# Performance work log

Measured on AMD Instinct MI355X. Metric: run time of the kernel, lower is better.

Reference implementation:

```python
import jax, jax.numpy as jnp
import numpy as np

N = 20000; E = 320000; INPUT_DIM = 512; HIDDEN = 128; OUT_DIM = 64
ORIGIN = 256; PRETRAIN = 256; HEADS = 8; DK = 16; DC = 256
MAX_POS = 512; NTRAIN = 200000


def setup_inputs():
    ks = jax.random.split(jax.random.key(0), 24)
    def p(i, shape):
        return jax.random.normal(ks[i], shape, dtype=jnp.float32) * 0.05
    z = lambda n: jnp.zeros((n,), jnp.float32)
    return {
        "x": jax.random.normal(ks[0], (N, INPUT_DIM), dtype=jnp.float32),
        "train_sample": jax.random.randint(ks[1], (NTRAIN, 2), 0, N),
        "data_feature": jax.random.normal(ks[2], (N, INPUT_DIM), dtype=jnp.float32),
        "adj": jax.random.randint(ks[3], (2, E), 0, N),
        "positions": jax.random.randint(ks[4], (N,), 0, MAX_POS),
        "gcn_W": p(5, (INPUT_DIM, ORIGIN)), "gcn_b": z(ORIGIN),
        "gcnA2_W": p(6, (INPUT_DIM, PRETRAIN)), "gcnA2_b": z(PRETRAIN),
        "lin_W": p(7, (ORIGIN, HIDDEN)), "lin_b": z(HIDDEN),
        "tf_W": p(8, (PRETRAIN, HIDDEN)), "tf_b": z(HIDDEN),
        "tg_W": p(9, (PRETRAIN, HIDDEN)), "tg_b": z(HIDDEN),
        "Wq": p(10, (HIDDEN, HEADS * DK)), "bq": z(HEADS * DK),
        "Wk": p(11, (HIDDEN, HEADS * DK)), "bk": z(HEADS * DK),
        "Wv": p(12, (HIDDEN, HEADS * DK)), "bv": z(HEADS * DK),
        "Wo": p(13, (HEADS * DK, HIDDEN)), "bo": z(HIDDEN),
        "Ek": p(14, (DC, N)), "Ev": p(15, (DC, N)),
        "pos_emb": p(16, (MAX_POS, HIDDEN)),
        "tfa_W": p(17, (HIDDEN, OUT_DIM)), "tfa_b": z(OUT_DIM),
        "tga_W": p(18, (HIDDEN, OUT_DIM)), "tga_b": z(OUT_DIM),
    }


def _leaky(v):
    return jnp.where(v >= 0, v, 0.01 * v)


def _gcn(x, W, b, src, dst):
    # PyG GCNConv: add self-loops, symmetric D^-1/2 (A+I) D^-1/2 normalization
    h = x @ W                                   # [N, F_out]
    deg = jnp.ones((N,), x.dtype).at[dst].add(1.0)   # degree incl. self-loop
    dinv = jax.lax.rsqrt(deg)
    coef = (dinv[src] * dinv[dst])[:, None]
    agg = jax.ops.segment_sum(h[src] * coef, dst, num_segments=N)
    return agg + h * (dinv * dinv)[:, None] + b


def _attention(q_in, k_in, v_in, positions, pos_emb, Wq, bq, Wk, bk, Wv, bv, Wo, bo, Ek, Ev):
    # Compressed (Linformer-style) multi-head attention over the node axis:
    # keys/values projected from N nodes down to DC landmarks (d_c=d_c_prime=256).
    pe = pos_emb[positions]                     # [N, HIDDEN]
    q = ((q_in + pe) @ Wq + bq).reshape(N, HEADS, DK)
    k = (k_in + pe) @ Wk + bk                   # [N, HEADS*DK]
    v = v_in @ Wv + bv
    kc = (Ek @ k).reshape(DC, HEADS, DK)        # [DC, H, DK]
    vc = (Ev @ v).reshape(DC, HEADS, DK)
    scores = jnp.einsum("nhd,chd->hnc", q, kc) / (DK ** 0.5)
    w = jax.nn.softmax(scores, axis=-1)         # [H, N, DC]
    out = jnp.einsum("hnc,chd->nhd", w, vc).reshape(N, HEADS * DK)
    return out @ Wo + bo                        # [N, HIDDEN]


def reference(x, train_sample, data_feature, adj, positions,
              gcn_W, gcn_b, gcnA2_W, gcnA2_b, lin_W, lin_b,
              tf_W, tf_b, tg_W, tg_b,
              Wq, bq, Wk, bk, Wv, bv, Wo, bo, Ek, Ev, pos_emb,
              tfa_W, tfa_b, tga_W, tga_b):
    src, dst = adj[0], adj[1]
    x_g = jax.nn.sigmoid(_gcn(data_feature, gcn_W, gcn_b, src, dst))
    x_g = _leaky(x_g @ lin_W + lin_b)
    x_a = _gcn(data_feature, gcnA2_W, gcnA2_b, src, dst)
    tf_embed = _leaky(x_a @ tf_W + tf_b)
    target_embed = _leaky(x_a @ tg_W + tg_b)
    x_f = _attention(x_g, tf_embed, target_embed, positions, pos_emb,
                     Wq, bq, Wk, bk, Wv, bv, Wo, bo, Ek, Ev)
    tfa = _leaky(x_f @ tfa_W + tfa_b)
    tga = _leaky(x_f @ tga_W + tga_b)
    a = tfa[train_sample[:, 0]]
    b = tga[train_sample[:, 1]]
    dot = jnp.sum(a * b, axis=1)
    denom = jnp.maximum(jnp.linalg.norm(a, axis=1) * jnp.linalg.norm(b, axis=1), 1e-8)
    return (dot / denom)[:, None]                # [NTRAIN, 1]
```

## Files before the change

### kernel.cpp

```cpp
#include <hip/hip_runtime.h>
#include <hip/hip_bf16.h>

#define N_NODES 20000
#define E_EDGES 320000
#define NTRAIN  200000
#define KC_SPLITS 64

template<int PRE, int POST>
__global__ __launch_bounds__(256) void gemm_f32(
    const float* __restrict__ A, const float* __restrict__ W,
    const float* __restrict__ bias, float* __restrict__ C,
    int M, int K, int Nn,
    const int* __restrict__ positions, const float* __restrict__ pos_emb)
{
    __shared__ float As[16][68];
    __shared__ float Bs[16][64];

    const int t  = threadIdx.x;
    const int m0 = blockIdx.x * 64;
    const int n0 = blockIdx.y * 64;

    const int kl  = t & 15;
    const int ml  = t >> 4;
    const int nl  = t & 63;
    const int kl2 = t >> 6;
    const int tc  = t & 15;
    const int tr  = t >> 4;

    float acc[4][4] = {};

    for (int k0 = 0; k0 < K; k0 += 16) {
        #pragma unroll
        for (int i = 0; i < 4; i++) {
            int row = m0 + ml + i * 16;
            float v = 0.f;
            if (row < M) {
                v = A[(size_t)row * K + k0 + kl];
                if (PRE == 1) v = 1.f / (1.f + expf(-v));
                if (PRE == 2) v += pos_emb[(size_t)positions[row] * K + k0 + kl];
            }
            As[kl][ml + i * 16] = v;
        }
        #pragma unroll
        for (int i = 0; i < 4; i++) {
            int kk = kl2 * 4 + i;
            Bs[kk][nl] = W[(size_t)(k0 + kk) * Nn + n0 + nl];
        }
        __syncthreads();
        #pragma unroll
        for (int kk = 0; kk < 16; kk++) {
            float4 ra = *reinterpret_cast<const float4*>(&As[kk][tr * 4]);
            float4 rb = *reinterpret_cast<const float4*>(&Bs[kk][tc * 4]);
            float am[4] = {ra.x, ra.y, ra.z, ra.w};
            float bn[4] = {rb.x, rb.y, rb.z, rb.w};
            #pragma unroll
            for (int i = 0; i < 4; i++)
                #pragma unroll
                for (int j = 0; j < 4; j++)
                    acc[i][j] += am[i] * bn[j];
        }
        __syncthreads();
    }

    #pragma unroll
    for (int i = 0; i < 4; i++) {
        int row = m0 + tr * 4 + i;
        if (row >= M) continue;
        #pragma unroll
        for (int j = 0; j < 4; j++) {
            int col = n0 + tc * 4 + j;
            float v = acc[i][j] + (bias ? bias[col] : 0.f);
            if (POST == 1) v = (v >= 0.f) ? v : 0.01f * v;
            C[(size_t)row * Nn + col] = v;
        }
    }
}

template<int PRE, int POST>
__global__ __launch_bounds__(256) void gemm_f32_n128(
    const float* __restrict__ A, const float* __restrict__ W,
    const float* __restrict__ bias, float* __restrict__ C,
    int M, int K, int Nn,
    const int* __restrict__ positions, const float* __restrict__ pos_emb)
{
    __shared__ float As[16][68];
    __shared__ float Bs[16][144];

    const int t  = threadIdx.x;
    const int m0 = blockIdx.x * 64;
    const int n0 = blockIdx.y * 128;

    const int kl = t & 15;
    const int ml = t >> 4;
    const int nl = t & 127;
    const int kb = t >> 7;

    const int tc = t & 15;
    const int tr = t >> 4;
    const int bPhys = tc * 8 + (tc >> 2) * 4;

    float acc[4][8] = {};

    for (int k0 = 0; k0 < K; k0 += 16) {
        #pragma unroll
        for (int i = 0; i < 4; i++) {
            int row = m0 + ml + i * 16;
            float v = 0.f;
            if (row < M) {
                v = A[(size_t)row * K + k0 + kl];
                if (PRE == 1) v = 1.f / (1.f + expf(-v));
                if (PRE == 2) v += pos_emb[(size_t)positions[row] * K + k0 + kl];
            }
            As[kl][ml + i * 16] = v;
        }
        {
            int pc = nl + (nl >> 5) * 4;
            #pragma unroll
            for (int i = 0; i < 8; i++) {
                int kk = kb + i * 2;
                Bs[kk][pc] = W[(size_t)(k0 + kk) * Nn + n0 + nl];
            }
        }
        __syncthreads();
        #pragma unroll
        for (int kk = 0; kk < 16; kk++) {
            float4 ra  = *reinterpret_cast<const float4*>(&As[kk][tr * 4]);
            float4 rb0 = *reinterpret_cast<const float4*>(&Bs[kk][bPhys]);
            float4 rb1 = *reinterpret_cast<const float4*>(&Bs[kk][bPhys + 4]);
            float am[4] = {ra.x, ra.y, ra.z, ra.w};
            float bn[8] = {rb0.x, rb0.y, rb0.z, rb0.w, rb1.x, rb1.y, rb1.z, rb1.w};
            #pragma unroll
            for (int i = 0; i < 4; i++)
                #pragma unroll
                for (int j = 0; j < 8; j++)
                    acc[i][j] += am[i] * bn[j];
        }
        __syncthreads();
    }

    #pragma unroll
    for (int i = 0; i < 4; i++) {
        int row = m0 + tr * 4 + i;
        if (row >= M) continue;
        float4 o0, o1;
        float* po0 = (float*)&o0;
        float* po1 = (float*)&o1;
        #pragma unroll
        for (int j = 0; j < 4; j++) {
            float v = acc[i][j] + (bias ? bias[n0 + tc * 8 + j] : 0.f);
            if (POST == 1) v = (v >= 0.f) ? v : 0.01f * v;
            po0[j] = v;
            float w = acc[i][j + 4] + (bias ? bias[n0 + tc * 8 + 4 + j] : 0.f);
            if (POST == 1) w = (w >= 0.f) ? w : 0.01f * w;
            po1[j] = w;
        }
        *reinterpret_cast<float4*>(&C[(size_t)row * Nn + n0 + tc * 8])     = o0;
        *reinterpret_cast<float4*>(&C[(size_t)row * Nn + n0 + tc * 8 + 4]) = o1;
    }
}

__global__ void zero_kernel(float* __restrict__ p, int n)
{
    int i = blockIdx.x * 256 + threadIdx.x;
    if (i < n) p[i] = 0.f;
}

__global__ void csr_count(const int* __restrict__ dst, int* __restrict__ count)
{
    int e = blockIdx.x * 256 + threadIdx.x;
    int stride = gridDim.x * 256;
    for (; e < E_EDGES; e += stride)
        atomicAdd(&count[dst[e]], 1);
}

__global__ __launch_bounds__(1024) void csr_scan(
    const int* __restrict__ count, int* __restrict__ rowptr,
    int* __restrict__ cursor, float* __restrict__ dinv)
{
    __shared__ int s[1024];
    const int t = threadIdx.x;
    int carry = 0;
    for (int base = 0; base < N_NODES; base += 1024) {
        int i = base + t;
        int v = (i < N_NODES) ? count[i] : 0;
        if (i < N_NODES) dinv[i] = rsqrtf(1.f + (float)v);
        s[t] = v;
        __syncthreads();
        for (int off = 1; off < 1024; off <<= 1) {
            int add = (t >= off) ? s[t - off] : 0;
            __syncthreads();
            s[t] += add;
            __syncthreads();
        }
        int incl  = s[t];
        int total = s[1023];
        if (i < N_NODES) {
            rowptr[i] = carry + incl - v;
            cursor[i] = carry + incl - v;
        }
        carry += total;
        __syncthreads();
    }
    if (t == 0) rowptr[N_NODES] = carry;
}

__global__ void csr_fill(const int* __restrict__ src, const int* __restrict__ dst,
                         int* __restrict__ cursor, int* __restrict__ srcs)
{
    int e = blockIdx.x * 256 + threadIdx.x;
    int stride = gridDim.x * 256;
    for (; e < E_EDGES; e += stride) {
        int slot = atomicAdd(&cursor[dst[e]], 1);
        srcs[slot] = src[e];
    }
}

__global__ __launch_bounds__(256) void gcn_aggregate(
    const float* __restrict__ H1, const float* __restrict__ H2,
    const float* __restrict__ dinv,
    const int* __restrict__ rowptr, const int* __restrict__ srcs,
    const float* __restrict__ b1, const float* __restrict__ b2,
    float* __restrict__ O1, float* __restrict__ O2)
{
    const int n = blockIdx.x;
    const int f = threadIdx.x;
    const float dn = dinv[n];
    const size_t nidx = (size_t)n * 256 + f;

    float a1 = H1[nidx] * dn * dn + b1[f];
    float a2 = H2[nidx] * dn * dn + b2[f];

    const int e0 = rowptr[n];
    const int e1 = rowptr[n + 1];
    for (int e = e0; e < e1; e++) {
        int s = srcs[e];
        float c = dinv[s] * dn;
        size_t si = (size_t)s * 256 + f;
        a1 += H1[si] * c;
        a2 += H2[si] * c;
    }
    O1[nidx] = a1;
    O2[nidx] = a2;
}

__global__ __launch_bounds__(256) void kcvc_kernel(
    const float* __restrict__ Ek, const float* __restrict__ Ev,
    const float* __restrict__ kin, const float* __restrict__ vin,
    float* __restrict__ partial)
{
    const float* E = blockIdx.z ? Ev  : Ek;
    const float* X = blockIdx.z ? vin : kin;

    const int c0 = blockIdx.x * 128;
    const int per = 320;
    const int nStart = blockIdx.y * per;
    const int nEnd   = min(nStart + per, N_NODES);

    __shared__ float Es[32][144];
    __shared__ float Xs[32][144];

    const int t  = threadIdx.x;
    const int tc = t & 15;
    const int td = t >> 4;
    const int ePhys = tc * 8 + (tc >> 2) * 4;
    const int xPhys = td * 8 + (td >> 2) * 4;

    float acc[8][8] = {};

    for (int nb = nStart; nb < nEnd; nb += 32) {
        const int nc = min(32, nEnd - nb);

        {
            int cl  = t >> 1;
            int pc  = cl + (cl >> 5) * 4;
            int nnb = (t & 1) * 16;
            const float* srcp = &E[(size_t)(c0 + cl) * N_NODES + nb + nnb];
            if (nc == 32) {
                #pragma unroll
                for (int i = 0; i < 4; i++) {
                    float4 v = *reinterpret_cast<const float4*>(&srcp[i * 4]);
                    Es[nnb + i * 4 + 0][pc] = v.x;
                    Es[nnb + i * 4 + 1][pc] = v.y;
                    Es[nnb + i * 4 + 2][pc] = v.z;
                    Es[nnb + i * 4 + 3][pc] = v.w;
                }
            } else {
                for (int i = 0; i < 16; i++) {
                    int nn = nnb + i;
                    Es[nn][pc] = (nn < nc) ? srcp[i] : 0.f;
                }
            }
        }
        {
            #pragma unroll
            for (int i = 0; i < 4; i++) {
                int g  = t + i * 256;
                int nn = g >> 5;
                int d0 = (g & 31) * 4;
                int pd = d0 + (d0 >> 5) * 4;
                if (nn < nc) {
                    float4 v = *reinterpret_cast<const float4*>(&X[(size_t)(nb + nn) * 128 + d0]);
                    Xs[nn][pd + 0] = v.x; Xs[nn][pd + 1] = v.y;
                    Xs[nn][pd + 2] = v.z; Xs[nn][pd + 3] = v.w;
                } else {
                    Xs[nn][pd + 0] = 0.f; Xs[nn][pd + 1] = 0.f;
                    Xs[nn][pd + 2] = 0.f; Xs[nn][pd + 3] = 0.f;
                }
            }
        }
        __syncthreads();

        #pragma unroll 2
        for (int nn = 0; nn < 32; nn++) {
            float4 e0 = *reinterpret_cast<const float4*>(&Es[nn][ePhys]);
            float4 e1 = *reinterpret_cast<const float4*>(&Es[nn][ePhys + 4]);
            float4 x0 = *reinterpret_cast<const float4*>(&Xs[nn][xPhys]);
            float4 x1 = *reinterpret_cast<const float4*>(&Xs[nn][xPhys + 4]);
            float ev[8] = {e0.x, e0.y, e0.z, e0.w, e1.x, e1.y, e1.z, e1.w};
            float xv[8] = {x0.x, x0.y, x0.z, x0.w, x1.x, x1.y, x1.z, x1.w};
            #pragma unroll
            for (int ci = 0; ci < 8; ci++)
                #pragma unroll
                for (int dj = 0; dj < 8; dj++)
                    acc[ci][dj] += ev[ci] * xv[dj];
        }
        __syncthreads();
    }

    float* pb = partial + ((size_t)(blockIdx.z * KC_SPLITS + blockIdx.y)) * 32768;
    #pragma unroll
    for (int ci = 0; ci < 8; ci++) {
        int c = c0 + tc * 8 + ci;
        float4 v0 = {acc[ci][0], acc[ci][1], acc[ci][2], acc[ci][3]};
        float4 v1 = {acc[ci][4], acc[ci][5], acc[ci][6], acc[ci][7]};
        *reinterpret_cast<float4*>(&pb[(size_t)c * 128 + td * 8])     = v0;
        *reinterpret_cast<float4*>(&pb[(size_t)c * 128 + td * 8 + 4]) = v1;
    }
}

__global__ __launch_bounds__(256) void kcvc_reduce(
    const float* __restrict__ partial, float* __restrict__ out)
{
    int i4  = blockIdx.x * 256 + threadIdx.x;
    int mat = i4 >> 13;
    int off = (i4 & 8191) * 4;
    const float* p = partial + (size_t)mat * KC_SPLITS * 32768 + off;
    float4 acc = {0.f, 0.f, 0.f, 0.f};
    #pragma unroll 8
    for (int s = 0; s < KC_SPLITS; s++) {
        float4 v = *reinterpret_cast<const float4*>(p + (size_t)s * 32768);
        acc.x += v.x; acc.y += v.y; acc.z += v.z; acc.w += v.w;
    }
    *reinterpret_cast<float4*>(out + (size_t)mat * 32768 + off) = acc;
}

__global__ __launch_bounds__(256) void attn_kernel(
    const float* __restrict__ q, const float* __restrict__ kc,
    const float* __restrict__ vc, float* __restrict__ outp)
{
    __shared__ float q_s[16][132];
    __shared__ float kc_s[16][272];
    __shared__ float vc_s[256][20];
    __shared__ float w_s[16][264];

    const int t    = threadIdx.x;
    const int n0   = blockIdx.x * 16;
    const int node = t >> 4;
    const int tn   = t & 15;

    {
        const float* qp = q + (size_t)n0 * 128;
        #pragma unroll
        for (int i = 0; i < 2; i++) {
            int idx = t * 8 + i * 4;
            float4 v = *reinterpret_cast<const float4*>(&qp[idx]);
            *reinterpret_cast<float4*>(&q_s[idx >> 7][idx & 127]) = v;
        }
    }

    for (int h = 0; h < 8; h++) {
        __syncthreads();
        {
            const float* kp = &kc[(size_t)t * 128 + h * 16];
            float4 a0 = *reinterpret_cast<const float4*>(kp);
            float4 a1 = *reinterpret_cast<const float4*>(kp + 4);
            float4 a2 = *reinterpret_cast<const float4*>(kp + 8);
            float4 a3 = *reinterpret_cast<const float4*>(kp + 12);
            kc_s[ 0][t] = a0.x; kc_s[ 1][t] = a0.y; kc_s[ 2][t] = a0.z; kc_s[ 3][t] = a0.w;
            kc_s[ 4][t] = a1.x; kc_s[ 5][t] = a1.y; kc_s[ 6][t] = a1.z; kc_s[ 7][t] = a1.w;
            kc_s[ 8][t] = a2.x; kc_s[ 9][t] = a2.y; kc_s[10][t] = a2.z; kc_s[11][t] = a2.w;
            kc_s[12][t] = a3.x; kc_s[13][t] = a3.y; kc_s[14][t] = a3.z; kc_s[15][t] = a3.w;
            const float* vp = &vc[(size_t)t * 128 + h * 16];
            *reinterpret_cast<float4*>(&vc_s[t][ 0]) = *reinterpret_cast<const float4*>(vp);
            *reinterpret_cast<float4*>(&vc_s[t][ 4]) = *reinterpret_cast<const float4*>(vp + 4);
            *reinterpret_cast<float4*>(&vc_s[t][ 8]) = *reinterpret_cast<const float4*>(vp + 8);
            *reinterpret_cast<float4*>(&vc_s[t][12]) = *reinterpret_cast<const float4*>(vp + 12);
        }
        __syncthreads();

        float qr[16];
        #pragma unroll
        for (int d = 0; d < 16; d++) qr[d] = q_s[node][h * 16 + d];

        float sv[16];
        #pragma unroll
        for (int j = 0; j < 16; j++) {
            int c = tn + 16 * j;
            float a = 0.f;
            #pragma unroll
            for (int d = 0; d < 16; d++)
                a += qr[d] * kc_s[d][c];
            sv[j] = a * 0.25f;
        }

        float m = sv[0];
        #pragma unroll
        for (int j = 1; j < 16; j++) m = fmaxf(m, sv[j]);
        #pragma unroll
        for (int off = 8; off > 0; off >>= 1)
            m = fmaxf(m, __shfl_xor(m, off));

        float sum = 0.f;
        #pragma unroll
        for (int j = 0; j < 16; j++) {
            sv[j] = expf(sv[j] - m);
            sum += sv[j];
        }
        #pragma unroll
        for (int off = 8; off > 0; off >>= 1)
            sum += __shfl_xor(sum, off);
        float inv = 1.0f / sum;

        #pragma unroll
        for (int j = 0; j < 16; j++)
            w_s[node][tn + 16 * j] = sv[j] * inv;
        __syncthreads();

        float acc0 = 0.f, acc1 = 0.f, acc2 = 0.f, acc3 = 0.f;
        #pragma unroll 4
        for (int cb = 0; cb < 64; cb++) {
            int c = cb * 4;
            float4 w4 = *reinterpret_cast<const float4*>(&w_s[node][c]);
            acc0 += w4.x * vc_s[c + 0][tn];
            acc1 += w4.y * vc_s[c + 1][tn];
            acc2 += w4.z * vc_s[c + 2][tn];
            acc3 += w4.w * vc_s[c + 3][tn];
        }
        outp[(size_t)(n0 + node) * 128 + h * 16 + tn] = (acc0 + acc1) + (acc2 + acc3);
    }
}

__global__ __launch_bounds__(256) void cosine_kernel(
    const float* __restrict__ tfa, const float* __restrict__ tga,
    const int* __restrict__ ts, float* __restrict__ out)
{
    const int w    = threadIdx.x >> 6;
    const int lane = threadIdx.x & 63;
    const int t    = blockIdx.x * 4 + w;
    if (t >= NTRAIN) return;

    int i = ts[2 * t];
    int j = ts[2 * t + 1];
    float a = tfa[(size_t)i * 64 + lane];
    float b = tga[(size_t)j * 64 + lane];
    float da = a * b, na = a * a, nb = b * b;
    #pragma unroll
    for (int off = 32; off > 0; off >>= 1) {
        da += __shfl_xor(da, off);
        na += __shfl_xor(na, off);
        nb += __shfl_xor(nb, off);
    }
    if (lane == 0)
        out[t] = da / fmaxf(sqrtf(na) * sqrtf(nb), 1e-8f);
}

extern "C" void kernel_launch(void* const* d_in, const int* in_sizes, int n_in,
                              void* d_out, int out_size, void* d_ws, size_t ws_size,
                              hipStream_t stream)
{
    const int*   ts    = (const int*)  d_in[1];
    const float* X     = (const float*)d_in[2];
    const int*   adj   = (const int*)  d_in[3];
    const int*   pos   = (const int*)  d_in[4];
    const float* gcn_W = (const float*)d_in[5];
    const float* gcn_b = (const float*)d_in[6];
    const float* gA2_W = (const float*)d_in[7];
    const float* gA2_b = (const float*)d_in[8];
    const float* lin_W = (const float*)d_in[9];
    const float* lin_b = (const float*)d_in[10];
    const float* tf_W  = (const float*)d_in[11];
    const float* tf_b  = (const float*)d_in[12];
    const float* tg_W  = (const float*)d_in[13];
    const float* tg_b  = (const float*)d_in[14];
    const float* Wq    = (const float*)d_in[15];
    const float* bq    = (const float*)d_in[16];
    const float* Wk    = (const float*)d_in[17];
    const float* bk    = (const float*)d_in[18];
    const float* Wv    = (const float*)d_in[19];
    const float* bv    = (const float*)d_in[20];
    const float* Wo    = (const float*)d_in[21];
    const float* bo    = (const float*)d_in[22];
    const float* Ek    = (const float*)d_in[23];
    const float* Ev    = (const float*)d_in[24];
    const float* pemb  = (const float*)d_in[25];
    const float* tfaW  = (const float*)d_in[26];
    const float* tfab  = (const float*)d_in[27];
    const float* tgaW  = (const float*)d_in[28];
    const float* tgab  = (const float*)d_in[29];

    const int* src = adj;
    const int* dst = adj + E_EDGES;

    float* ws  = (float*)d_ws;
    float* H1  = ws;
    float* H2  = H1 + 5120000;
    float* O1  = H2 + 5120000;
    float* O2  = O1 + 5120000;
    float* dinv = O2 + 5120000;
    float* kc  = dinv + 20000;
    float* vc  = kc + 32768;
    int*   count  = (int*)(vc + 32768);
    int*   rowptr = count + 20000;
    int*   cursor = rowptr + 20001;
    int*   srcs   = cursor + 20000;
    float* xg   = H1;
    float* tfe  = H1 + 2560000;
    float* tge  = H2;
    float* qb   = H2 + 2560000;
    float* kb   = O1;
    float* vb   = O1 + 2560000;
    float* attn = O2;
    float* xf   = O2 + 2560000;
    float* tfa  = H1;
    float* tga  = H1 + 1280000;
    float* partial = H1;

    dim3 blk(256);
    const int MB = (N_NODES + 63) / 64;

    gemm_f32_n128<0,0><<<dim3(MB,2), blk, 0, stream>>>(X, gcn_W, nullptr, H1, N_NODES, 512, 256, nullptr, nullptr);
    gemm_f32_n128<0,0><<<dim3(MB,2), blk, 0, stream>>>(X, gA2_W, nullptr, H2, N_NODES, 512, 256, nullptr, nullptr);

    zero_kernel<<<(20000 + 255) / 256, blk, 0, stream>>>((float*)count, 20000);
    csr_count<<<1250, blk, 0, stream>>>(dst, count);
    csr_scan<<<1, 1024, 0, stream>>>(count, rowptr, cursor, dinv);
    csr_fill<<<1250, blk, 0, stream>>>(src, dst, cursor, srcs);

    gcn_aggregate<<<N_NODES, blk, 0, stream>>>(H1, H2, dinv, rowptr, srcs,
                                               gcn_b, gA2_b, O1, O2);

    gemm_f32_n128<1,1><<<dim3(MB,1), blk, 0, stream>>>(O1, lin_W, lin_b, xg, N_NODES, 256, 128, nullptr, nullptr);
    gemm_f32_n128<0,1><<<dim3(MB,1), blk, 0, stream>>>(O2, tf_W, tf_b, tfe, N_NODES, 256, 128, nullptr, nullptr);
    gemm_f32_n128<0,1><<<dim3(MB,1), blk, 0, stream>>>(O2, tg_W, tg_b, tge, N_NODES, 256, 128, nullptr, nullptr);

    gemm_f32_n128<2,0><<<dim3(MB,1), blk, 0, stream>>>(xg,  Wq, bq, qb, N_NODES, 128, 128, pos, pemb);
    gemm_f32_n128<2,0><<<dim3(MB,1), blk, 0, stream>>>(tfe, Wk, bk, kb, N_NODES, 128, 128, pos, pemb);
    gemm_f32_n128<0,0><<<dim3(MB,1), blk, 0, stream>>>(tge, Wv, bv, vb, N_NODES, 128, 128, nullptr, nullptr);

    kcvc_kernel<<<dim3(2, KC_SPLITS, 2), blk, 0, stream>>>(Ek, Ev, kb, vb, partial);
    kcvc_reduce<<<64, blk, 0, stream>>>(partial, kc);

    attn_kernel<<<1250, blk, 0, stream>>>(qb, kc, vc, attn);

    gemm_f32_n128<0,0><<<dim3(MB,1), blk, 0, stream>>>(attn, Wo, bo, xf, N_NODES, 128, 128, nullptr, nullptr);

    gemm_f32<0,1><<<dim3(MB,1), blk, 0, stream>>>(xf, tfaW, tfab, tfa, N_NODES, 128, 64, nullptr, nullptr);
    gemm_f32<0,1><<<dim3(MB,1), blk, 0, stream>>>(xf, tgaW, tgab, tga, N_NODES, 128, 64, nullptr, nullptr);

    cosine_kernel<<<NTRAIN / 4, blk, 0, stream>>>(tfa, tga, ts, (float*)d_out);
}
```

Baseline: 1.076 ms.

## Retile kcvc to 64-row blocks and register-tile attention scores

```diff
diff --git a/kernel.cpp b/kernel.cpp
--- a/kernel.cpp
+++ b/kernel.cpp
@@ -251,45 +251,32 @@
     const float* E = blockIdx.z ? Ev  : Ek;
     const float* X = blockIdx.z ? vin : kin;
 
-    const int c0 = blockIdx.x * 128;
+    const int c0 = blockIdx.x * 64;
     const int per = 320;
     const int nStart = blockIdx.y * per;
     const int nEnd   = min(nStart + per, N_NODES);
 
-    __shared__ float Es[32][144];
+    __shared__ float Es[32][68];
     __shared__ float Xs[32][144];
 
     const int t  = threadIdx.x;
     const int tc = t & 15;
     const int td = t >> 4;
-    const int ePhys = tc * 8 + (tc >> 2) * 4;
     const int xPhys = td * 8 + (td >> 2) * 4;
 
-    float acc[8][8] = {};
+    float acc[4][8] = {};
 
     for (int nb = nStart; nb < nEnd; nb += 32) {
-        const int nc = min(32, nEnd - nb);
-
         {
-            int cl  = t >> 1;
-            int pc  = cl + (cl >> 5) * 4;
-            int nnb = (t & 1) * 16;
+            int cl  = t >> 2;
+            int nnb = (t & 3) * 8;
             const float* srcp = &E[(size_t)(c0 + cl) * N_NODES + nb + nnb];
-            if (nc == 32) {
-                #pragma unroll
-                for (int i = 0; i < 4; i++) {
-                    float4 v = *reinterpret_cast<const float4*>(&srcp[i * 4]);
-                    Es[nnb + i * 4 + 0][pc] = v.x;
-                    Es[nnb + i * 4 + 1][pc] = v.y;
-                    Es[nnb + i * 4 + 2][pc] = v.z;
-                    Es[nnb + i * 4 + 3][pc] = v.w;
-                }
-            } else {
-                for (int i = 0; i < 16; i++) {
-                    int nn = nnb + i;
-                    Es[nn][pc] = (nn < nc) ? srcp[i] : 0.f;
-                }
-            }
+            float4 v0 = *reinterpret_cast<const float4*>(&srcp[0]);
+            float4 v1 = *reinterpret_cast<const float4*>(&srcp[4]);
+            Es[nnb + 0][cl] = v0.x; Es[nnb + 1][cl] = v0.y;
+            Es[nnb + 2][cl] = v0.z; Es[nnb + 3][cl] = v0.w;
+            Es[nnb + 4][cl] = v1.x; Es[nnb + 5][cl] = v1.y;
+            Es[nnb + 6][cl] = v1.z; Es[nnb + 7][cl] = v1.w;
         }
         {
             #pragma unroll
@@ -298,28 +285,22 @@
                 int nn = g >> 5;
                 int d0 = (g & 31) * 4;
                 int pd = d0 + (d0 >> 5) * 4;
-                if (nn < nc) {
-                    float4 v = *reinterpret_cast<const float4*>(&X[(size_t)(nb + nn) * 128 + d0]);
-                    Xs[nn][pd + 0] = v.x; Xs[nn][pd + 1] = v.y;
-                    Xs[nn][pd + 2] = v.z; Xs[nn][pd + 3] = v.w;
-                } else {
-                    Xs[nn][pd + 0] = 0.f; Xs[nn][pd + 1] = 0.f;
-                    Xs[nn][pd + 2] = 0.f; Xs[nn][pd + 3] = 0.f;
-                }
+                float4 v = *reinterpret_cast<const float4*>(&X[(size_t)(nb + nn) * 128 + d0]);
+                Xs[nn][pd + 0] = v.x; Xs[nn][pd + 1] = v.y;
+                Xs[nn][pd + 2] = v.z; Xs[nn][pd + 3] = v.w;
             }
         }
         __syncthreads();
 
         #pragma unroll 2
         for (int nn = 0; nn < 32; nn++) {
-            float4 e0 = *reinterpret_cast<const float4*>(&Es[nn][ePhys]);
-            float4 e1 = *reinterpret_cast<const float4*>(&Es[nn][ePhys + 4]);
+            float4 e4 = *reinterpret_cast<const float4*>(&Es[nn][tc * 4]);
             float4 x0 = *reinterpret_cast<const float4*>(&Xs[nn][xPhys]);
             float4 x1 = *reinterpret_cast<const float4*>(&Xs[nn][xPhys + 4]);
-            float ev[8] = {e0.x, e0.y, e0.z, e0.w, e1.x, e1.y, e1.z, e1.w};
+            float ev[4] = {e4.x, e4.y, e4.z, e4.w};
             float xv[8] = {x0.x, x0.y, x0.z, x0.w, x1.x, x1.y, x1.z, x1.w};
             #pragma unroll
-            for (int ci = 0; ci < 8; ci++)
+            for (int ci = 0; ci < 4; ci++)
                 #pragma unroll
                 for (int dj = 0; dj < 8; dj++)
                     acc[ci][dj] += ev[ci] * xv[dj];
@@ -327,10 +308,10 @@
         __syncthreads();
     }
 
-    float* pb = partial + ((size_t)(blockIdx.z * KC_SPLITS + blockIdx.y)) * 32768;
+    float* pb = partial + (size_t)(blockIdx.z * KC_SPLITS + blockIdx.y) * 32768;
     #pragma unroll
-    for (int ci = 0; ci < 8; ci++) {
-        int c = c0 + tc * 8 + ci;
+    for (int ci = 0; ci < 4; ci++) {
+        int c = c0 + tc * 4 + ci;
         float4 v0 = {acc[ci][0], acc[ci][1], acc[ci][2], acc[ci][3]};
         float4 v1 = {acc[ci][4], acc[ci][5], acc[ci][6], acc[ci][7]};
         *reinterpret_cast<float4*>(&pb[(size_t)c * 128 + td * 8])     = v0;
@@ -359,12 +340,14 @@
     const float* __restrict__ vc, float* __restrict__ outp)
 {
     __shared__ float q_s[16][132];
-    __shared__ float kc_s[16][272];
-    __shared__ float vc_s[256][20];
-    __shared__ float w_s[16][264];
+    __shared__ float kc_s[16][260];
+    __shared__ float vc_s[16][260];
+    __shared__ float w_s[16][260];
 
     const int t    = threadIdx.x;
     const int n0   = blockIdx.x * 16;
+    const int ng   = t >> 6;
+    const int tc2  = t & 63;
     const int node = t >> 4;
     const int tn   = t & 15;
 
@@ -391,62 +374,84 @@
             kc_s[ 8][t] = a2.x; kc_s[ 9][t] = a2.y; kc_s[10][t] = a2.z; kc_s[11][t] = a2.w;
             kc_s[12][t] = a3.x; kc_s[13][t] = a3.y; kc_s[14][t] = a3.z; kc_s[15][t] = a3.w;
             const float* vp = &vc[(size_t)t * 128 + h * 16];
-            *reinterpret_cast<float4*>(&vc_s[t][ 0]) = *reinterpret_cast<const float4*>(vp);
-            *reinterpret_cast<float4*>(&vc_s[t][ 4]) = *reinterpret_cast<const float4*>(vp + 4);
-            *reinterpret_cast<float4*>(&vc_s[t][ 8]) = *reinterpret_cast<const float4*>(vp + 8);
-            *reinterpret_cast<float4*>(&vc_s[t][12]) = *reinterpret_cast<const float4*>(vp + 12);
-        }
-        __syncthreads();
-
-        float qr[16];
-        #pragma unroll
-        for (int d = 0; d < 16; d++) qr[d] = q_s[node][h * 16 + d];
-
-        float sv[16];
-        #pragma unroll
-        for (int j = 0; j < 16; j++) {
-            int c = tn + 16 * j;
-            float a = 0.f;
-            #pragma unroll
-            for (int d = 0; d < 16; d++)
-                a += qr[d] * kc_s[d][c];
-            sv[j] = a * 0.25f;
-        }
-
-        float m = sv[0];
-        #pragma unroll
-        for (int j = 1; j < 16; j++) m = fmaxf(m, sv[j]);
-        #pragma unroll
-        for (int off = 8; off > 0; off >>= 1)
-            m = fmaxf(m, __shfl_xor(m, off));
-
-        float sum = 0.f;
-        #pragma unroll
-        for (int j = 0; j < 16; j++) {
-            sv[j] = expf(sv[j] - m);
-            sum += sv[j];
-        }
-        #pragma unroll
-        for (int off = 8; off > 0; off >>= 1)
-            sum += __shfl_xor(sum, off);
-        float inv = 1.0f / sum;
-
-        #pragma unroll
-        for (int j = 0; j < 16; j++)
-            w_s[node][tn + 16 * j] = sv[j] * inv;
-        __syncthreads();
-
-        float acc0 = 0.f, acc1 = 0.f, acc2 = 0.f, acc3 = 0.f;
-        #pragma unroll 4
-        for (int cb = 0; cb < 64; cb++) {
-            int c = cb * 4;
-            float4 w4 = *reinterpret_cast<const float4*>(&w_s[node][c]);
-            acc0 += w4.x * vc_s[c + 0][tn];
-            acc1 += w4.y * vc_s[c + 1][tn];
-            acc2 += w4.z * vc_s[c + 2][tn];
-            acc3 += w4.w * vc_s[c + 3][tn];
-        }
-        outp[(size_t)(n0 + node) * 128 + h * 16 + tn] = (acc0 + acc1) + (acc2 + acc3);
+            float4 b0 = *reinterpret_cast<const float4*>(vp);
+            float4 b1 = *reinterpret_cast<const float4*>(vp + 4);
+            float4 b2 = *reinterpret_cast<const float4*>(vp + 8);
+            float4 b3 = *reinterpret_cast<const float4*>(vp + 12);
+            vc_s[ 0][t] = b0.x; vc_s[ 1][t] = b0.y; vc_s[ 2][t] = b0.z; vc_s[ 3][t] = b0.w;
+            vc_s[ 4][t] = b1.x; vc_s[ 5][t] = b1.y; vc_s[ 6][t] = b1.z; vc_s[ 7][t] = b1.w;
+            vc_s[ 8][t] = b2.x; vc_s[ 9][t] = b2.y; vc_s[10][t] = b2.z; vc_s[11][t] = b2.w;
+            vc_s[12][t] = b3.x; vc_s[13][t] = b3.y; vc_s[14][t] = b3.z; vc_s[15][t] = b3.w;
+        }
+        __syncthreads();
+
+        float qreg[4][16];
+        #pragma unroll
+        for (int j = 0; j < 4; j++)
+            #pragma unroll
+            for (int dq = 0; dq < 4; dq++) {
+                float4 qv = *reinterpret_cast<const float4*>(&q_s[4 * ng + j][h * 16 + 4 * dq]);
+                qreg[j][4 * dq + 0] = qv.x; qreg[j][4 * dq + 1] = qv.y;
+                qreg[j][4 * dq + 2] = qv.z; qreg[j][4 * dq + 3] = qv.w;
+            }
+
+        float sv[4][4] = {};
+        #pragma unroll
+        for (int d = 0; d < 16; d++) {
+            float4 kv = *reinterpret_cast<const float4*>(&kc_s[d][4 * tc2]);
+            float kvv[4] = {kv.x, kv.y, kv.z, kv.w};
+            #pragma unroll
+            for (int j = 0; j < 4; j++)
+                #pragma unroll
+                for (int i = 0; i < 4; i++)
+                    sv[j][i] += qreg[j][d] * kvv[i];
+        }
+
+        float mx[4], sm[4];
+        #pragma unroll
+        for (int j = 0; j < 4; j++) {
+            #pragma unroll
+            for (int i = 0; i < 4; i++) sv[j][i] *= 0.25f;
+            mx[j] = fmaxf(fmaxf(sv[j][0], sv[j][1]), fmaxf(sv[j][2], sv[j][3]));
+        }
+        #pragma unroll
+        for (int off = 32; off > 0; off >>= 1)
+            #pragma unroll
+            for (int j = 0; j < 4; j++)
+                mx[j] = fmaxf(mx[j], __shfl_xor(mx[j], off));
+        #pragma unroll
+        for (int j = 0; j < 4; j++) {
+            sm[j] = 0.f;
+            #pragma unroll
+            for (int i = 0; i < 4; i++) {
+                sv[j][i] = expf(sv[j][i] - mx[j]);
+                sm[j] += sv[j][i];
+            }
+        }
+        #pragma unroll
+        for (int off = 32; off > 0; off >>= 1)
+            #pragma unroll
+            for (int j = 0; j < 4; j++)
+                sm[j] += __shfl_xor(sm[j], off);
+        #pragma unroll
+        for (int j = 0; j < 4; j++) {
+            float inv = 1.0f / sm[j];
+            float4 wv = {sv[j][0] * inv, sv[j][1] * inv, sv[j][2] * inv, sv[j][3] * inv};
+            *reinterpret_cast<float4*>(&w_s[4 * ng + j][4 * tc2]) = wv;
+        }
+        __syncthreads();
+
+        float a0 = 0.f, a1 = 0.f, a2 = 0.f, a3 = 0.f;
+        #pragma unroll 8
+        for (int i = 0; i < 64; i++) {
+            float4 w4 = *reinterpret_cast<const float4*>(&w_s[node][4 * i]);
+            float4 v4 = *reinterpret_cast<const float4*>(&vc_s[tn][4 * i]);
+            a0 += w4.x * v4.x;
+            a1 += w4.y * v4.y;
+            a2 += w4.z * v4.z;
+            a3 += w4.w * v4.w;
+        }
+        outp[(size_t)(n0 + node) * 128 + h * 16 + tn] = (a0 + a1) + (a2 + a3);
     }
 }
 
@@ -557,7 +562,7 @@
     gemm_f32_n128<2,0><<<dim3(MB,1), blk, 0, stream>>>(tfe, Wk, bk, kb, N_NODES, 128, 128, pos, pemb);
     gemm_f32_n128<0,0><<<dim3(MB,1), blk, 0, stream>>>(tge, Wv, bv, vb, N_NODES, 128, 128, nullptr, nullptr);
 
-    kcvc_kernel<<<dim3(2, KC_SPLITS, 2), blk, 0, stream>>>(Ek, Ev, kb, vb, partial);
+    kcvc_kernel<<<dim3(4, KC_SPLITS, 2), blk, 0, stream>>>(Ek, Ev, kb, vb, partial);
     kcvc_reduce<<<64, blk, 0, stream>>>(partial, kc);
 
     attn_kernel<<<1250, blk, 0, stream>>>(qb, kc, vc, attn);
```

After: 1.051 ms. 1.02x faster.
